# Performance work log

Hardware: AMD Instinct MI355X
Metric: run time of the kernel (lower is better)

## Reference

```python
import jax, jax.numpy as jnp
import numpy as np

# Dims (see shape_source): resolution H must equal H_sp, W_sp must be 1 for the
# module's reshapes/broadcasts to be consistent.
B, HRES, WRES = 2, 4, 8192
H_SP, W_SP, H_SEC = 4, 1, 4          # window height, window width, sector height
C, NH = 512, 8
HD = C // NH
L = HRES * WRES                       # 32768 query tokens
NS = H_SEC * WRES                     # sector tokens (from k.view(B,C,H,W))
NW = B * (HRES // H_SP) * (WRES // W_SP)  # number of windows = B*WRES
SCALE = HD ** -0.5
EPS = 1e-5


def setup_inputs() -> dict:
    key = jax.random.key(0)
    ks = jax.random.split(key, 12)
    f32 = jnp.float32
    rn = lambda k, shp, s=1.0: jax.random.normal(k, shp, dtype=f32) * s
    return {
        "s": rn(ks[0], (B, NS, C)),
        "x": rn(ks[1], (B, L, C)),
        "s_pos": rn(ks[2], (B, H_SEC * W_SP, WRES // W_SP, 2)),
        "x_pos": rn(ks[3], (B, L, 2)),
        "Wq": rn(ks[4], (C, C), 0.02), "bq": jnp.zeros((C,), f32),
        "Wk": rn(ks[5], (C, C), 0.02), "bk": jnp.zeros((C,), f32),
        "Wv": rn(ks[6], (C, C), 0.02), "bv": jnp.zeros((C,), f32),
        "pw1": rn(ks[7], (16, 2), 0.3), "pb1": jnp.zeros((16,), f32),
        "bn_g": jnp.ones((16,), f32), "bn_b": jnp.zeros((16,), f32),
        "bn_m": jnp.zeros((16,), f32), "bn_v": jnp.ones((16,), f32),
        "pw2": rn(ks[8], (NH, 16), 0.3), "pb2": jnp.zeros((NH,), f32),
    }


def reference(s, x, s_pos, x_pos, Wq, bq, Wk, bk, Wv, bv,
              pw1, pb1, bn_g, bn_b, bn_m, bn_v, pw2, pb2):
    # ---- relative position bias (pointwise conv1d + BN(eval) + ReLU + conv1d) ----
    xp = x_pos.reshape(B, HRES // H_SP, H_SP, WRES // W_SP, W_SP, 2)
    xp = jnp.transpose(xp, (0, 1, 3, 5, 2, 4)).reshape(-1, 2, H_SP * W_SP)   # [NW,2,4]
    sp = jnp.transpose(s_pos, (0, 2, 3, 1)).reshape(-1, 2, H_SEC * W_SP)      # [NW,2,4]
    rel = xp[:, :, :, None] - sp[:, :, None, :]                               # [NW,2,4,4]
    rel = rel.reshape(NW, 2, -1)                                              # [NW,2,16]
    h = jnp.einsum('oc,ncl->nol', pw1, rel) + pb1[None, :, None]
    h = (h - bn_m[None, :, None]) * jax.lax.rsqrt(bn_v[None, :, None] + EPS)
    h = h * bn_g[None, :, None] + bn_b[None, :, None]
    h = jax.nn.relu(h)
    bias = jnp.einsum('oc,ncl->nol', pw2, h) + pb2[None, :, None]
    bias = bias.reshape(NW, NH, H_SP * W_SP, H_SEC * W_SP)                    # [NW,NH,4,4]

    # ---- q: im2cswin (true transpose to [B,C,H,W], then window partition) ----
    q = x @ Wq + bq                                                           # [B,L,C]
    q = jnp.transpose(q, (0, 2, 1)).reshape(B, C, HRES // H_SP, H_SP, WRES // W_SP, W_SP)
    q = jnp.transpose(q, (0, 2, 4, 3, 5, 1)).reshape(NW, H_SP * W_SP, NH, HD)
    q = jnp.transpose(q, (0, 2, 1, 3))                                        # [NW,NH,4,HD]

    # ---- k,v: raw view(B,C,H_sec,W) as in torch (memory reinterp, NOT transpose) ----
    def sector_windows(t):
        t = t.reshape(B, C, H_SEC, WRES)
        t = t.reshape(B, NH, HD, H_SEC, WRES // W_SP, W_SP)
        t = jnp.transpose(t, (0, 4, 1, 3, 5, 2))                              # [B,W,NH,Hs,Wsp,HD]
        return t.reshape(NW, NH, H_SEC * W_SP, HD)
    k = sector_windows(s @ Wk + bk)
    v = sector_windows(s @ Wv + bv)

    # ---- windowed attention with bias ----
    attn = jnp.einsum('nhqd,nhkd->nhqk', q * SCALE, k) + bias
    attn = jax.nn.softmax(attn, axis=-1)
    o = jnp.einsum('nhqk,nhkd->nhqd', attn, v)
    o = jnp.transpose(o, (0, 2, 1, 3)).reshape(NW, H_SP * W_SP, C)

    # ---- windows2img ----
    o = o.reshape(B, HRES // H_SP, WRES // W_SP, H_SP, W_SP, C)
    o = jnp.transpose(o, (0, 1, 3, 2, 4, 5)).reshape(B, L, C)
    return o
```

## Files before the change

kernel.cpp:

```cpp
#include <hip/hip_runtime.h>


typedef unsigned short u16;
typedef unsigned int u32;
typedef __attribute__((ext_vector_type(8))) short bf16x8;
typedef __attribute__((ext_vector_type(4))) float f32x4;
typedef __attribute__((ext_vector_type(8))) unsigned short u16x8;
typedef __attribute__((ext_vector_type(4))) unsigned short u16x4;
typedef __attribute__((ext_vector_type(4))) unsigned int u32x4;

__device__ __forceinline__ u16 f2b(float f) {
  u32 u = __float_as_uint(f);
  return (u16)((u + 0x7FFFu + ((u >> 16) & 1u)) >> 16);
}
__device__ __forceinline__ float b2f(u16 v) { return __uint_as_float(((u32)v) << 16); }
__device__ __forceinline__ float b2f_lo(u32 d) { return __uint_as_float(d << 16); }
__device__ __forceinline__ float b2f_hi(u32 d) { return __uint_as_float(d & 0xffff0000u); }
__device__ __forceinline__ u32 cvt_pk(float lo, float hi) {
  u32 r;
  asm("v_cvt_pk_bf16_f32 %0, %1, %2" : "=v"(r) : "v"(lo), "v"(hi));
  return r;
}
#define GLDS(g, l)                                                                     \
  __builtin_amdgcn_global_load_lds((const __attribute__((address_space(1))) void*)(g), \
                                   (__attribute__((address_space(3))) void*)(l), 16, 0, 0)
#define SBAR() __builtin_amdgcn_sched_barrier(0)

__global__ __launch_bounds__(256) void prep_kernel(
    const float* __restrict__ Wq, const float* __restrict__ Wk, const float* __restrict__ Wv,
    u16* __restrict__ Wt, const float* __restrict__ s, u16* __restrict__ sb,
    const float* __restrict__ xpos, const float* __restrict__ spos,
    const float* __restrict__ pw1, const float* __restrict__ pb1,
    const float* __restrict__ bng, const float* __restrict__ bnb,
    const float* __restrict__ bnm, const float* __restrict__ bnv,
    const float* __restrict__ pw2, const float* __restrict__ pb2, float* __restrict__ biasw) {
  int bid = (int)blockIdx.x;
  int t = threadIdx.x;
  if (bid < 16384) {
    size_t i = ((size_t)bid * 256 + t) * 8;
    float4 v0 = *(const float4*)(s + i);
    float4 v1 = *(const float4*)(s + i + 4);
    u32x4 pk;
    pk[0] = cvt_pk(v0.x, v0.y);
    pk[1] = cvt_pk(v0.z, v0.w);
    pk[2] = cvt_pk(v1.x, v1.y);
    pk[3] = cvt_pk(v1.z, v1.w);
    *(u32x4*)(sb + i) = pk;
  } else if (bid < 19456) {
    int r = bid - 16384;
    int mat = r >> 10, bx = r & 1023;
    const float* W = (mat == 0) ? Wq : (mat == 1) ? Wk : Wv;
    int g = bx * 256 + t;
    int n = g >> 9, k = g & 511;
    Wt[(size_t)mat * 262144 + g] = f2b(W[k * 512 + n]);
  } else {
    int bx = bid - 19456;
    int wl = t & 63, p = t >> 6;
    int n = bx * 64 + wl;
    int b = n >> 13, w = n & 8191;
    float Am[16], Bm[16], Cm[16];
#pragma unroll
    for (int m = 0; m < 16; ++m) {
      float scv = bng[m] * rsqrtf(bnv[m] + 1e-5f);
      Am[m] = pw1[2 * m] * scv;
      Bm[m] = pw1[2 * m + 1] * scv;
      Cm[m] = (pb1[m] - bnm[m]) * scv + bnb[m];
    }
    size_t xi = ((size_t)(b * 32768 + p * 8192 + w)) * 2;
    float xp0 = xpos[xi], xp1 = xpos[xi + 1];
#pragma unroll
    for (int ks = 0; ks < 4; ++ks) {
      size_t si = ((size_t)((b * 4 + ks) * 8192 + w)) * 2;
      float r0 = xp0 - spos[si];
      float r1 = xp1 - spos[si + 1];
      float o[8];
#pragma unroll
      for (int oo = 0; oo < 8; ++oo) o[oo] = pb2[oo];
#pragma unroll
      for (int m = 0; m < 16; ++m) {
        float h = fmaxf(Am[m] * r0 + Bm[m] * r1 + Cm[m], 0.f);
#pragma unroll
        for (int oo = 0; oo < 8; ++oo) o[oo] += pw2[oo * 16 + m] * h;
      }
#pragma unroll
      for (int oo = 0; oo < 8; ++oo)
        biasw[((size_t)(((b * 8 + oo) * 4 + p) * 4 + ks)) * 8192 + w] = o[oo];
    }
  }
}

__global__ __launch_bounds__(256, 3) void gemm_kernel(const float* __restrict__ A,
                                                      const u16* __restrict__ Bt,
                                                      const float* __restrict__ biasv,
                                                      u16* __restrict__ Out) {
  __shared__ u16 lds[24576];
  const int t = threadIdx.x, lane = t & 63, wv = t >> 6;
  const int id = (int)blockIdx.x;
  const int lg = (id & 7) * 256 + (id >> 3);
  const int mt = (lg >> 2) * 128, nt = (lg & 3) * 128;
  const int fr = lane & 15, kg = lane >> 4;
  const int wm = (wv & 1) * 64, wn = (wv >> 1) * 64;

  const int arow = lane >> 3;
  const int agr = (lane & 7) ^ arow;
  const int brow = lane >> 2;
  const int bgr = (lane & 3) ^ (brow & 3) ^ ((brow >> 2) & 3);

  const float* Abase = A + (size_t)mt * 512;
  const u16* Bbase = Bt + (size_t)nt * 512;

  f32x4 acc[4][4];
#pragma unroll
  for (int i = 0; i < 4; ++i)
#pragma unroll
    for (int j = 0; j < 4; ++j) acc[i][j] = (f32x4){0.f, 0.f, 0.f, 0.f};

#define STAGEQ(buf, kt)                                                       \
  {                                                                           \
    u16* Ab_ = lds + (buf)*8192;                                              \
    u16* Bb_ = lds + 16384 + (buf)*4096;                                      \
    _Pragma("unroll") for (int ii = 0; ii < 4; ++ii) {                        \
      int inst = wv * 4 + ii;                                                 \
      GLDS(Abase + (size_t)(inst * 8 + arow) * 512 + (kt) + agr * 4,          \
           Ab_ + inst * 512);                                                 \
    }                                                                         \
    _Pragma("unroll") for (int ii = 0; ii < 2; ++ii) {                        \
      int inst = wv * 2 + ii;                                                 \
      GLDS(Bbase + (size_t)(inst * 16 + brow) * 512 + (kt) + bgr * 8,         \
           Bb_ + inst * 512);                                                 \
    }                                                                         \
  }

  STAGEQ(0, 0);

  for (int ki = 0; ki < 16; ++ki) {
    int cur = ki & 1;
    if (ki < 15) {
      STAGEQ(cur ^ 1, (ki + 1) * 32);
      asm volatile("s_waitcnt vmcnt(6)" ::: "memory");
    } else {
      asm volatile("s_waitcnt vmcnt(0)" ::: "memory");
    }
    SBAR();
    __builtin_amdgcn_s_barrier();
    SBAR();

    const u16* Ab = lds + cur * 8192;
    const u16* Bb = lds + 16384 + cur * 4096;
    bf16x8 af[4], bfr[4];
#pragma unroll
    for (int i = 0; i < 4; ++i) {
      int r = wm + i * 16 + fr;
      int p0 = (2 * kg) ^ (r & 7), p1 = p0 ^ 1;
      f32x4 a0 = *(const f32x4*)&Ab[r * 64 + p0 * 8];
      f32x4 a1 = *(const f32x4*)&Ab[r * 64 + p1 * 8];
      union { bf16x8 v; u32 w[4]; } uu;
      uu.w[0] = cvt_pk(a0[0], a0[1]);
      uu.w[1] = cvt_pk(a0[2], a0[3]);
      uu.w[2] = cvt_pk(a1[0], a1[1]);
      uu.w[3] = cvt_pk(a1[2], a1[3]);
      af[i] = uu.v;
    }
#pragma unroll
    for (int j = 0; j < 4; ++j) {
      int r = wn + j * 16 + fr;
      int pos = kg ^ (r & 3) ^ ((r >> 2) & 3);
      bfr[j] = *(const bf16x8*)&Bb[r * 32 + pos * 8];
    }
    __builtin_amdgcn_s_setprio(1);
#pragma unroll
    for (int i = 0; i < 4; ++i)
#pragma unroll
      for (int j = 0; j < 4; ++j)
        acc[i][j] = __builtin_amdgcn_mfma_f32_16x16x32_bf16(af[i], bfr[j], acc[i][j], 0, 0, 0);
    __builtin_amdgcn_s_setprio(0);

    SBAR();
    __builtin_amdgcn_s_barrier();
    SBAR();
  }
#undef STAGEQ

  u16* Clds = lds;
#pragma unroll
  for (int i = 0; i < 4; ++i)
#pragma unroll
    for (int r = 0; r < 4; ++r) {
      int row = wm + i * 16 + kg * 4 + r;
#pragma unroll
      for (int j = 0; j < 4; ++j) {
        int ch = wn + j * 16 + fr;
        Clds[row * 136 + ch] = f2b(acc[i][j][r] + biasv[nt + ch]);
      }
    }
  __syncthreads();
#pragma unroll
  for (int c = 0; c < 8; ++c) {
    int off = c * 2048 + t * 8;
    int row = off >> 7, col = off & 127;
    *(u16x8*)(Out + (size_t)(mt + row) * 512 + nt + col) = *(const u16x8*)&Clds[row * 136 + col];
  }
}

__global__ __launch_bounds__(512, 4) void fused_attn_kernel(
    const u16* __restrict__ sb, const u16* __restrict__ WtK, const u16* __restrict__ WtV,
    const float* __restrict__ bK, const float* __restrict__ bV,
    const u16* __restrict__ Qt, const float* __restrict__ biasw, float* __restrict__ out) {
  __shared__ __align__(16) char LDS[74752];
  float* Xf = (float*)LDS;
  float* alds = (float*)(LDS + 4096);
  u16* Klds = (u16*)(LDS + 8192);
  u16* Vlds = (u16*)(LDS + 40960);

  const int t = threadIdx.x, lane = t & 63, wv = t >> 6;
  const int i0 = (int)blockIdx.x;
  const int xcd = i0 & 7, qq = i0 >> 3;
  const int g = (qq >> 6) * 8 + xcd, inner = qq & 63;
  const int b = g >> 4, u = g & 15;
  const int cg = inner >> 3, nh = inner & 7;
  const int fr = lane & 15, kg = lane >> 4;
  const int p3p = wv >> 1, dh = wv & 1;
  const int mg = wv >> 1, ng = wv & 1;

  f32x4 accK[4][2], accV[4][2];
#pragma unroll
  for (int i = 0; i < 4; ++i)
#pragma unroll
    for (int j = 0; j < 2; ++j) {
      accK[i][j] = (f32x4){0.f, 0.f, 0.f, 0.f};
      accV[i][j] = (f32x4){0.f, 0.f, 0.f, 0.f};
    }

  const int lgr = (lane & 3) ^ ((lane >> 3) & 3);

#define STAGEF(buf, kt)                                                                 \
  {                                                                                     \
    u16* Sb_ = (u16*)(LDS) + (buf)*8192;                                                \
    _Pragma("unroll") for (int ii = 0; ii < 2; ++ii) {                                  \
      int i = wv * 2 + ii;                                                              \
      int r = i * 16 + (lane >> 2);                                                     \
      int grow = nh * 4096 + (r >> 2) * 64 + (r & 3) * 16 + u;                          \
      GLDS(sb + (size_t)(b * 32768 + grow) * 512 + (kt) + lgr * 8, Sb_ + i * 512);      \
    }                                                                                   \
    {                                                                                   \
      const u16* wsrc = (wv < 4) ? WtK : WtV;                                           \
      u16* Wb_ = (u16*)(LDS + 49152 + (buf)*8192 + ((wv < 4) ? 0 : 4096));              \
      int i = wv & 3;                                                                   \
      int r = i * 16 + (lane >> 2);                                                     \
      GLDS(wsrc + (size_t)(cg * 64 + r) * 512 + (kt) + lgr * 8, Wb_ + i * 512);         \
    }                                                                                   \
  }

  STAGEF(0, 0);
  STAGEF(1, 32);

  for (int ki = 0; ki < 16; ++ki) {
    int cur = ki % 3;
    if (ki < 15) {
      asm volatile("s_waitcnt vmcnt(3)" ::: "memory");
    } else {
      asm volatile("s_waitcnt vmcnt(0)" ::: "memory");
    }
    SBAR();
    __builtin_amdgcn_s_barrier();
    SBAR();

    const u16* Sb = (const u16*)(LDS) + cur * 8192;
    const u16* Kb = (const u16*)(LDS + 49152 + cur * 8192);
    const u16* Vb = (const u16*)(LDS + 49152 + cur * 8192 + 4096);
    bf16x8 af[4];
#pragma unroll
    for (int i = 0; i < 4; ++i) {
      int r = mg * 64 + i * 16 + fr;
      int gpos = kg ^ ((fr >> 1) & 3);
      af[i] = *(const bf16x8*)&Sb[r * 32 + gpos * 8];
    }
    {
      bf16x8 bkf[2];
#pragma unroll
      for (int j = 0; j < 2; ++j) {
        int r = ng * 32 + j * 16 + fr;
        int gpos = kg ^ ((fr >> 1) & 3);
        bkf[j] = *(const bf16x8*)&Kb[r * 32 + gpos * 8];
      }
      __builtin_amdgcn_s_setprio(1);
#pragma unroll
      for (int i = 0; i < 4; ++i)
#pragma unroll
        for (int j = 0; j < 2; ++j)
          accK[i][j] = __builtin_amdgcn_mfma_f32_16x16x32_bf16(af[i], bkf[j], accK[i][j], 0, 0, 0);
      __builtin_amdgcn_s_setprio(0);
    }
    {
      bf16x8 bvf[2];
#pragma unroll
      for (int j = 0; j < 2; ++j) {
        int r = ng * 32 + j * 16 + fr;
        int gpos = kg ^ ((fr >> 1) & 3);
        bvf[j] = *(const bf16x8*)&Vb[r * 32 + gpos * 8];
      }
      __builtin_amdgcn_s_setprio(1);
#pragma unroll
      for (int i = 0; i < 4; ++i)
#pragma unroll
        for (int j = 0; j < 2; ++j)
          accV[i][j] = __builtin_amdgcn_mfma_f32_16x16x32_bf16(af[i], bvf[j], accV[i][j], 0, 0, 0);
      __builtin_amdgcn_s_setprio(0);
    }
    SBAR();
    if (ki < 14) STAGEF((ki + 2) % 3, (ki + 2) * 32);
    SBAR();
  }
#undef STAGEF

  SBAR();
  float bkr[2], bvr[2];
#pragma unroll
  for (int j = 0; j < 2; ++j) {
    bkr[j] = bK[cg * 64 + ng * 32 + j * 16 + fr];
    bvr[j] = bV[cg * 64 + ng * 32 + j * 16 + fr];
  }
  u32x4 qv[4];
  {
    const u16* qp =
        Qt + (size_t)(b * 32768 + p3p * 8192 + u * 512 + cg * 64 + lane) * 512 + nh * 64 + dh * 32;
#pragma unroll
    for (int i = 0; i < 4; ++i) qv[i] = *(const u32x4*)(qp + i * 8);
  }
  float br[4];
  {
    const size_t bb = ((size_t)((b * 8 + nh) * 16 + p3p * 4)) * 8192 + u * 512 + cg * 64 + lane;
#pragma unroll
    for (int ks = 0; ks < 4; ++ks) br[ks] = biasw[bb + (size_t)ks * 8192];
  }
  SBAR();
  __builtin_amdgcn_s_barrier();
  SBAR();

#pragma unroll
  for (int i = 0; i < 4; ++i) {
    int d = mg * 16 + i * 4 + kg;
    int row0 = mg * 64 + i * 16 + kg * 4;
#pragma unroll
    for (int j = 0; j < 2; ++j) {
      int col = ng * 32 + j * 16 + fr;
      u16x4 kq, vq;
#pragma unroll
      for (int rr = 0; rr < 4; ++rr) {
        kq[rr] = f2b(accK[i][j][rr] + bkr[j]);
        vq[rr] = f2b(accV[i][j][rr] + bvr[j]);
      }
      *(u16x4*)&Klds[(d * 64 + col) * 4] = kq;
      *(u16x4*)&Vlds[col * 264 + row0] = vq;
    }
  }
  __syncthreads();

  float sc[4] = {0.f, 0.f, 0.f, 0.f};
#pragma unroll
  for (int dd = 0; dd < 32; ++dd) {
    int d = dh * 32 + dd;
    u32 word = qv[dd >> 3][(dd >> 1) & 3];
    float qd = (dd & 1) ? b2f_hi(word) : b2f_lo(word);
    u16x4 kv4 = *(const u16x4*)&Klds[(d * 64 + lane) * 4];
#pragma unroll
    for (int ks = 0; ks < 4; ++ks) sc[ks] += qd * b2f(kv4[ks]);
  }
  if (dh == 1) {
#pragma unroll
    for (int ks = 0; ks < 4; ++ks) Xf[(p3p * 4 + ks) * 64 + lane] = sc[ks];
  }
  __syncthreads();

  if (dh == 0) {
    float sv[4];
#pragma unroll
    for (int ks = 0; ks < 4; ++ks)
      sv[ks] = (sc[ks] + Xf[(p3p * 4 + ks) * 64 + lane]) * 0.125f + br[ks];
    float mx = fmaxf(fmaxf(sv[0], sv[1]), fmaxf(sv[2], sv[3]));
    float e0 = __expf(sv[0] - mx), e1 = __expf(sv[1] - mx), e2 = __expf(sv[2] - mx),
          e3 = __expf(sv[3] - mx);
    float inv = 1.f / (e0 + e1 + e2 + e3);
#pragma unroll
    for (int ks = 0; ks < 4; ++ks) {
      float e = (ks == 0) ? e0 : (ks == 1) ? e1 : (ks == 2) ? e2 : e3;
      alds[(p3p * 4 + ks) * 64 + lane] = e * inv;
    }
  }
  __syncthreads();

  float* ob = out + (size_t)(b * 32768 + p3p * 8192 + u * 512 + cg * 64) * 512 + nh * 64 + lane;
#pragma unroll
  for (int cc = 0; cc < 32; ++cc) {
    int c = dh * 32 + cc;
    u16x4 vvv = *(const u16x4*)&Vlds[c * 264 + lane * 4];
    float a0 = alds[(p3p * 4 + 0) * 64 + c];
    float a1 = alds[(p3p * 4 + 1) * 64 + c];
    float a2 = alds[(p3p * 4 + 2) * 64 + c];
    float a3 = alds[(p3p * 4 + 3) * 64 + c];
    float o = a0 * b2f(vvv[0]) + a1 * b2f(vvv[1]) + a2 * b2f(vvv[2]) + a3 * b2f(vvv[3]);
    ob[(size_t)c * 512] = o;
  }
}

extern "C" void kernel_launch(void* const* d_in, const int* in_sizes, int n_in,
                              void* d_out, int out_size, void* d_ws, size_t ws_size,
                              hipStream_t stream) {
  (void)in_sizes; (void)n_in; (void)out_size; (void)ws_size;
  const float* s     = (const float*)d_in[0];
  const float* x     = (const float*)d_in[1];
  const float* s_pos = (const float*)d_in[2];
  const float* x_pos = (const float*)d_in[3];
  const float* Wq = (const float*)d_in[4];  const float* bq = (const float*)d_in[5];
  const float* Wk = (const float*)d_in[6];  const float* bk = (const float*)d_in[7];
  const float* Wv = (const float*)d_in[8];  const float* bv = (const float*)d_in[9];
  const float* pw1 = (const float*)d_in[10]; const float* pb1 = (const float*)d_in[11];
  const float* bng = (const float*)d_in[12]; const float* bnb = (const float*)d_in[13];
  const float* bnm = (const float*)d_in[14]; const float* bnv = (const float*)d_in[15];
  const float* pw2 = (const float*)d_in[16]; const float* pb2 = (const float*)d_in[17];
  float* out = (float*)d_out;

  char* ws = (char*)d_ws;
  u16* Qt = (u16*)ws;
  float* biasw = (float*)(ws + 67108864);
  u16* Wt = (u16*)(ws + 75497472);
  u16* sbuf = (u16*)(ws + 77070336);

  prep_kernel<<<dim3(19712), 256, 0, stream>>>(Wq, Wk, Wv, Wt, s, sbuf, x_pos, s_pos, pw1, pb1,
                                               bng, bnb, bnm, bnv, pw2, pb2, biasw);
  gemm_kernel<<<dim3(2048), 256, 0, stream>>>(x, Wt, bq, Qt);
  fused_attn_kernel<<<dim3(2048), 512, 0, stream>>>(sbuf, Wt + 262144, Wt + 524288, bk, bv,
                                                    Qt, biasw, out);
}
```

Baseline: 238.5 us.

## Merge s-cast and bias prep into Q GEMM launch; issue attention prefetch earlier

Splits the weight transpose into its own small kernel and folds the s-to-bf16 conversion and position-bias computation into extra blocks of the Q projection GEMM launch. Those memory-bound blocks can then run alongside the compute-bound GEMM tiles instead of in a separate serial launch. Inside the fused attention loop, the stage for iteration ki+2 is now issued right after the barrier rather than after the MFMAs, to overlap more load latency. The merged kernel carries the GEMM's LDS allocation and launch bounds for every block, which may limit occupancy of the elementwise blocks.

```diff
diff --git a/kernel.cpp b/kernel.cpp
--- a/kernel.cpp
+++ b/kernel.cpp
@@ -26,77 +26,80 @@
                                    (__attribute__((address_space(3))) void*)(l), 16, 0, 0)
 #define SBAR() __builtin_amdgcn_sched_barrier(0)
 
-__global__ __launch_bounds__(256) void prep_kernel(
-    const float* __restrict__ Wq, const float* __restrict__ Wk, const float* __restrict__ Wv,
-    u16* __restrict__ Wt, const float* __restrict__ s, u16* __restrict__ sb,
+__global__ __launch_bounds__(256) void wt_kernel(const float* __restrict__ Wq,
+                                                 const float* __restrict__ Wk,
+                                                 const float* __restrict__ Wv,
+                                                 u16* __restrict__ Wt) {
+  int bid = (int)blockIdx.x;
+  int mat = bid >> 10, bx = bid & 1023;
+  const float* W = (mat == 0) ? Wq : (mat == 1) ? Wk : Wv;
+  int g = bx * 256 + threadIdx.x;
+  int n = g >> 9, k = g & 511;
+  Wt[(size_t)mat * 262144 + g] = f2b(W[k * 512 + n]);
+}
+
+__global__ __launch_bounds__(256, 3) void mid_kernel(
+    const float* __restrict__ A, const u16* __restrict__ Bt, const float* __restrict__ biasv,
+    u16* __restrict__ Out, const float* __restrict__ s, u16* __restrict__ sb,
     const float* __restrict__ xpos, const float* __restrict__ spos,
     const float* __restrict__ pw1, const float* __restrict__ pb1,
     const float* __restrict__ bng, const float* __restrict__ bnb,
     const float* __restrict__ bnm, const float* __restrict__ bnv,
     const float* __restrict__ pw2, const float* __restrict__ pb2, float* __restrict__ biasw) {
-  int bid = (int)blockIdx.x;
-  int t = threadIdx.x;
-  if (bid < 16384) {
-    size_t i = ((size_t)bid * 256 + t) * 8;
-    float4 v0 = *(const float4*)(s + i);
-    float4 v1 = *(const float4*)(s + i + 4);
-    u32x4 pk;
-    pk[0] = cvt_pk(v0.x, v0.y);
-    pk[1] = cvt_pk(v0.z, v0.w);
-    pk[2] = cvt_pk(v1.x, v1.y);
-    pk[3] = cvt_pk(v1.z, v1.w);
-    *(u32x4*)(sb + i) = pk;
-  } else if (bid < 19456) {
-    int r = bid - 16384;
-    int mat = r >> 10, bx = r & 1023;
-    const float* W = (mat == 0) ? Wq : (mat == 1) ? Wk : Wv;
-    int g = bx * 256 + t;
-    int n = g >> 9, k = g & 511;
-    Wt[(size_t)mat * 262144 + g] = f2b(W[k * 512 + n]);
-  } else {
-    int bx = bid - 19456;
-    int wl = t & 63, p = t >> 6;
-    int n = bx * 64 + wl;
-    int b = n >> 13, w = n & 8191;
-    float Am[16], Bm[16], Cm[16];
-#pragma unroll
-    for (int m = 0; m < 16; ++m) {
-      float scv = bng[m] * rsqrtf(bnv[m] + 1e-5f);
-      Am[m] = pw1[2 * m] * scv;
-      Bm[m] = pw1[2 * m + 1] * scv;
-      Cm[m] = (pb1[m] - bnm[m]) * scv + bnb[m];
-    }
-    size_t xi = ((size_t)(b * 32768 + p * 8192 + w)) * 2;
-    float xp0 = xpos[xi], xp1 = xpos[xi + 1];
-#pragma unroll
-    for (int ks = 0; ks < 4; ++ks) {
-      size_t si = ((size_t)((b * 4 + ks) * 8192 + w)) * 2;
-      float r0 = xp0 - spos[si];
-      float r1 = xp1 - spos[si + 1];
-      float o[8];
-#pragma unroll
-      for (int oo = 0; oo < 8; ++oo) o[oo] = pb2[oo];
+  __shared__ u16 lds[24576];
+  const int bid = (int)blockIdx.x;
+  const int t = threadIdx.x;
+
+  if (bid >= 2048) {
+    if (bid < 18432) {
+      size_t i = ((size_t)(bid - 2048) * 256 + t) * 8;
+      float4 v0 = *(const float4*)(s + i);
+      float4 v1 = *(const float4*)(s + i + 4);
+      u32x4 pk;
+      pk[0] = cvt_pk(v0.x, v0.y);
+      pk[1] = cvt_pk(v0.z, v0.w);
+      pk[2] = cvt_pk(v1.x, v1.y);
+      pk[3] = cvt_pk(v1.z, v1.w);
+      *(u32x4*)(sb + i) = pk;
+    } else {
+      int bx = bid - 18432;
+      int wl = t & 63, p = t >> 6;
+      int n = bx * 64 + wl;
+      int b = n >> 13, w = n & 8191;
+      float Am[16], Bm[16], Cm[16];
 #pragma unroll
       for (int m = 0; m < 16; ++m) {
-        float h = fmaxf(Am[m] * r0 + Bm[m] * r1 + Cm[m], 0.f);
-#pragma unroll
-        for (int oo = 0; oo < 8; ++oo) o[oo] += pw2[oo * 16 + m] * h;
-      }
-#pragma unroll
-      for (int oo = 0; oo < 8; ++oo)
-        biasw[((size_t)(((b * 8 + oo) * 4 + p) * 4 + ks)) * 8192 + w] = o[oo];
-    }
-  }
-}
-
-__global__ __launch_bounds__(256, 3) void gemm_kernel(const float* __restrict__ A,
-                                                      const u16* __restrict__ Bt,
-                                                      const float* __restrict__ biasv,
-                                                      u16* __restrict__ Out) {
-  __shared__ u16 lds[24576];
-  const int t = threadIdx.x, lane = t & 63, wv = t >> 6;
-  const int id = (int)blockIdx.x;
-  const int lg = (id & 7) * 256 + (id >> 3);
+        float scv = bng[m] * rsqrtf(bnv[m] + 1e-5f);
+        Am[m] = pw1[2 * m] * scv;
+        Bm[m] = pw1[2 * m + 1] * scv;
+        Cm[m] = (pb1[m] - bnm[m]) * scv + bnb[m];
+      }
+      size_t xi = ((size_t)(b * 32768 + p * 8192 + w)) * 2;
+      float xp0 = xpos[xi], xp1 = xpos[xi + 1];
+#pragma unroll
+      for (int ks = 0; ks < 4; ++ks) {
+        size_t si = ((size_t)((b * 4 + ks) * 8192 + w)) * 2;
+        float r0 = xp0 - spos[si];
+        float r1 = xp1 - spos[si + 1];
+        float o[8];
+#pragma unroll
+        for (int oo = 0; oo < 8; ++oo) o[oo] = pb2[oo];
+#pragma unroll
+        for (int m = 0; m < 16; ++m) {
+          float h = fmaxf(Am[m] * r0 + Bm[m] * r1 + Cm[m], 0.f);
+#pragma unroll
+          for (int oo = 0; oo < 8; ++oo) o[oo] += pw2[oo * 16 + m] * h;
+        }
+#pragma unroll
+        for (int oo = 0; oo < 8; ++oo)
+          biasw[((size_t)(((b * 8 + oo) * 4 + p) * 4 + ks)) * 8192 + w] = o[oo];
+      }
+    }
+    return;
+  }
+
+  const int lane = t & 63, wv = t >> 6;
+  const int lg = (bid & 7) * 256 + (bid >> 3);
   const int mt = (lg >> 2) * 128, nt = (lg & 3) * 128;
   const int fr = lane & 15, kg = lane >> 4;
   const int wm = (wv & 1) * 64, wn = (wv >> 1) * 64;
@@ -264,6 +267,8 @@
     SBAR();
     __builtin_amdgcn_s_barrier();
     SBAR();
+    if (ki < 14) STAGEF((ki + 2) % 3, (ki + 2) * 32);
+    SBAR();
 
     const u16* Sb = (const u16*)(LDS) + cur * 8192;
     const u16* Kb = (const u16*)(LDS + 49152 + cur * 8192);
@@ -307,8 +312,6 @@
           accV[i][j] = __builtin_amdgcn_mfma_f32_16x16x32_bf16(af[i], bvf[j], accV[i][j], 0, 0, 0);
       __builtin_amdgcn_s_setprio(0);
     }
-    SBAR();
-    if (ki < 14) STAGEF((ki + 2) % 3, (ki + 2) * 32);
     SBAR();
   }
 #undef STAGEF
@@ -426,9 +429,9 @@
   u16* Wt = (u16*)(ws + 75497472);
   u16* sbuf = (u16*)(ws + 77070336);
 
-  prep_kernel<<<dim3(19712), 256, 0, stream>>>(Wq, Wk, Wv, Wt, s, sbuf, x_pos, s_pos, pw1, pb1,
-                                               bng, bnb, bnm, bnv, pw2, pb2, biasw);
-  gemm_kernel<<<dim3(2048), 256, 0, stream>>>(x, Wt, bq, Qt);
+  wt_kernel<<<dim3(3072), 256, 0, stream>>>(Wq, Wk, Wv, Wt);
+  mid_kernel<<<dim3(18688), 256, 0, stream>>>(x, Wt, bq, Qt, s, sbuf, x_pos, s_pos, pw1, pb1,
+                                              bng, bnb, bnm, bnv, pw2, pb2, biasw);
   fused_attn_kernel<<<dim3(2048), 512, 0, stream>>>(sbuf, Wt + 262144, Wt + 524288, bk, bv,
                                                     Qt, biasw, out);
 }
```

Result: faster. 217.8 us (median of 2 runs) (-8.7%).
